# Kernel tuning notes

Hardware: AMD Instinct MI355X
Metric: run time of the kernel (lower is better)

## Reference

```python
import jax, jax.numpy as jnp
import numpy as np
from jax import lax

EPS = 1e-8


def setup_inputs() -> dict:
    key = jax.random.key(0)
    k1, k2, k3, k4, k5 = jax.random.split(key, 5)
    b, c_in, c_out, h, w_sp, k, z = 8, 256, 256, 128, 128, 3, 512
    return {
        "x": jax.random.normal(k1, (b, c_in, h, w_sp), dtype=jnp.float32),
        "w": jax.random.normal(k2, (b, z), dtype=jnp.float32),
        "weight": jax.random.normal(k3, (c_out, c_in, k, k), dtype=jnp.float32),
        "affine_w": jax.random.normal(k4, (c_in, z), dtype=jnp.float32) * 0.02,
        "affine_b": jax.random.normal(k5, (c_in,), dtype=jnp.float32) * 0.02,
    }


def reference(x, w, weight, affine_w, affine_b):
    # style: [b, c_in] -> broadcast over (out_ch, kh, kw); +1 as in StyleGAN2
    style = w @ affine_w.T + affine_b + 1.0                      # [b, c_in]
    wgt = weight[None] * style[:, None, :, None, None]           # [b, O, I, kh, kw]
    # demodulation
    denom = lax.rsqrt(jnp.sum(wgt * wgt, axis=(2, 3, 4)) + EPS)  # [b, O]
    wgt = wgt * denom[:, :, None, None, None]

    # per-sample conv (equivalent to groups=b grouped conv), 'same' padding
    def conv_one(xi, wi):
        # xi: [I, H, W], wi: [O, I, kh, kw]
        return lax.conv_general_dilated(
            xi[None], wi, window_strides=(1, 1), padding="SAME",
            dimension_numbers=("NCHW", "OIHW", "NCHW"))[0]

    return jax.vmap(conv_one)(x, wgt)                            # [b, O, H, W]
```

## Files before the change

### kernel.cpp

```cpp
#include <hip/hip_runtime.h>

#define EPS 1e-8f

using short8 = __attribute__((ext_vector_type(8))) short;
using f32x16 = __attribute__((ext_vector_type(16))) float;
typedef unsigned short u16;

#define WAITV(N) asm volatile("s_waitcnt vmcnt(" #N ")" ::: "memory")
#define BARRIER() do { __builtin_amdgcn_s_barrier(); \
                       asm volatile("" ::: "memory"); } while (0)

__device__ __forceinline__ u16 f2bf(float f) {
    union { float f; unsigned u; } v; v.f = f;
    unsigned u = v.u;
    return (u16)((u + 0x7FFFu + ((u >> 16) & 1u)) >> 16);
}

__device__ __forceinline__ void g2l16(const void* gsrc, void* ldst) {
    __builtin_amdgcn_global_load_lds(
        (const __attribute__((address_space(1))) unsigned int*)gsrc,
        (__attribute__((address_space(3))) unsigned int*)ldst, 16, 0, 0);
}

__global__ void style_kernel(const float* __restrict__ w,
                             const float* __restrict__ affine_w,
                             const float* __restrict__ affine_b,
                             float* __restrict__ style) {
    int b = blockIdx.x;
    int i = threadIdx.x;
    __shared__ float wb[512];
    for (int z = threadIdx.x; z < 512; z += 256) wb[z] = w[b * 512 + z];
    __syncthreads();
    const float* aw = affine_w + i * 512;
    float acc = 0.f;
#pragma unroll 4
    for (int z = 0; z < 512; z += 4) {
        float4 a4 = *reinterpret_cast<const float4*>(aw + z);
        acc += a4.x * wb[z] + a4.y * wb[z + 1] + a4.z * wb[z + 2] + a4.w * wb[z + 3];
    }
    style[b * 256 + i] = acc + affine_b[i] + 1.0f;
}

__global__ void modw_kernel(const float* __restrict__ weight,
                            const float* __restrict__ style,
                            u16* __restrict__ wgt) {
    int b = blockIdx.x >> 8;
    int o = blockIdx.x & 255;
    int ic = threadIdx.x;
    float s = style[b * 256 + ic];
    const float* wp = weight + (size_t)(o * 256 + ic) * 9;
    float m[9];
    float ss = 0.f;
#pragma unroll
    for (int t = 0; t < 9; ++t) { m[t] = wp[t] * s; ss += m[t] * m[t]; }
#pragma unroll
    for (int off = 32; off > 0; off >>= 1) ss += __shfl_down(ss, off);
    __shared__ float part[4];
    int lane = threadIdx.x & 63, wid = threadIdx.x >> 6;
    if (lane == 0) part[wid] = ss;
    __syncthreads();
    float denom = rsqrtf(part[0] + part[1] + part[2] + part[3] + EPS);
    int g = ic >> 3, j = ic & 7;
#pragma unroll
    for (int t = 0; t < 9; ++t) {
        size_t idx = ((((size_t)(b * 9 + t) * 32 + g) * 256 + o) << 3) + j;
        wgt[idx] = f2bf(m[t] * denom);
    }
}

__global__ __launch_bounds__(256) void xform_kernel(const float* __restrict__ x,
                                                    u16* __restrict__ xb) {
    int s = blockIdx.x * 256 + threadIdx.x;
    int w = s & 127, h = (s >> 7) & 127, g = (s >> 14) & 31, b = s >> 19;
    const float* xp = x + (((size_t)(b * 256 + g * 8) * 128 + h) * 128 + w);
    union { u16 u[8]; short8 v; } pk;
#pragma unroll
    for (int j = 0; j < 8; ++j) pk.u[j] = f2bf(xp[(size_t)j * 16384]);
    *reinterpret_cast<short8*>(&xb[(size_t)s * 8]) = pk.v;
}

__global__ __launch_bounds__(256, 2) void conv_kernel(
    const u16* __restrict__ xb,
    const u16* __restrict__ wgt,
    float* __restrict__ out) {

    __shared__ __align__(16) u16 Xs[2][4][4][130][8];
    __shared__ __align__(16) u16 trash[1024];

    int bid = blockIdx.x;
    int swz = (bid & 7) * 128 + (bid >> 3);
    int ht = swz & 63, ot = (swz >> 6) & 1, b = swz >> 7;
    int h0 = ht * 2;

    int tid = threadIdx.x, lane = tid & 63, wid = tid >> 6;
    int wm = wid >> 1, wr = wid & 1;
    int l31 = lane & 31, lh = lane >> 5;

    int hr = h0 + wid - 1;
    bool hValid = ((unsigned)hr < 128u);
    int hc = hValid ? hr : 0;

    const u16* aBase = wgt + ((size_t)(b * 9) * 32 * 256 +
                              (size_t)(lh * 256 + ot * 128 + wm * 64 + l31)) * 8;

    auto loadA = [&](short8 dst[2][2], int c, int t) {
#pragma unroll
        for (int kk = 0; kk < 2; ++kk)
#pragma unroll
            for (int mi = 0; mi < 2; ++mi)
                dst[kk][mi] = *reinterpret_cast<const short8*>(
                    aBase + (size_t)(((t * 32) + c * 4 + kk * 2) * 256 + mi * 32) * 8);
    };
    auto stageX = [&](int c1, int bx) {
#pragma unroll
        for (int k = 0; k < 8; ++k) {
            int g = k >> 1, half = k & 1;
            const u16* src = xb +
                ((((size_t)(b * 32 + c1 * 4 + g)) * 128 + hc) * 128 + half * 64 + lane) * 8;
            void* dst = hValid ? (void*)&Xs[bx][wid][g][1 + half * 64][0] : (void*)trash;
            g2l16(src, dst);
        }
    };

    {
        short8 z = {0, 0, 0, 0, 0, 0, 0, 0};
        short8* p0 = reinterpret_cast<short8*>(&Xs[0][0][0][0][0]);
        for (int i = tid; i < 4160; i += 256) p0[i] = z;
    }
    __syncthreads();

    short8 afC[2][2], afN[2][2];
    stageX(0, 0);
    loadA(afC, 0, 0);
    WAITV(4);
    BARRIER();

    f32x16 acc[2][4] = {};

    for (int c = 0; c < 8; ++c) {
        int buf = c & 1;
#pragma unroll
        for (int t = 0; t < 9; ++t) {
            if (!(c == 7 && t == 8))
                loadA(afN, t < 8 ? c : c + 1, t < 8 ? t + 1 : 0);
            if (t == 0 && c < 7) stageX(c + 1, buf ^ 1);

            int kh = t / 3, kw = t - kh * 3;
            short8 bx8[2][4];
#pragma unroll
            for (int kk = 0; kk < 2; ++kk)
#pragma unroll
                for (int ni = 0; ni < 4; ++ni)
                    bx8[kk][ni] = *reinterpret_cast<const short8*>(
                        &Xs[buf][wr + kh][kk * 2 + lh][ni * 32 + l31 + kw][0]);
            __builtin_amdgcn_s_setprio(1);
#pragma unroll
            for (int mi = 0; mi < 2; ++mi)
#pragma unroll
                for (int ni = 0; ni < 4; ++ni)
#pragma unroll
                    for (int kk = 0; kk < 2; ++kk)
                        acc[mi][ni] = __builtin_amdgcn_mfma_f32_32x32x16_bf16(
                            afC[kk][mi], bx8[kk][ni], acc[mi][ni], 0, 0, 0);
            __builtin_amdgcn_s_setprio(0);
#pragma unroll
            for (int kk = 0; kk < 2; ++kk)
#pragma unroll
                for (int mi = 0; mi < 2; ++mi)
                    afC[kk][mi] = afN[kk][mi];
        }
        WAITV(4);
        BARRIER();
    }

    int h = h0 + wr;
#pragma unroll
    for (int mi = 0; mi < 2; ++mi) {
        int ob = ot * 128 + wm * 64 + mi * 32 + 4 * lh;
#pragma unroll
        for (int ni = 0; ni < 4; ++ni) {
            int w_ = ni * 32 + l31;
#pragma unroll
            for (int reg = 0; reg < 16; ++reg) {
                int o = ob + (reg & 3) + 8 * (reg >> 2);
                out[(((size_t)(b * 256 + o) * 128 + h) * 128) + w_] = acc[mi][ni][reg];
            }
        }
    }
}

extern "C" void kernel_launch(void* const* d_in, const int* in_sizes, int n_in,
                              void* d_out, int out_size, void* d_ws, size_t ws_size,
                              hipStream_t stream) {
    const float* x        = (const float*)d_in[0];
    const float* w        = (const float*)d_in[1];
    const float* weight   = (const float*)d_in[2];
    const float* affine_w = (const float*)d_in[3];
    const float* affine_b = (const float*)d_in[4];
    float* out = (float*)d_out;

    float* style = (float*)d_ws;
    u16* wgt = (u16*)((char*)d_ws + 8192);
    u16* xbuf = (u16*)((char*)d_ws + 8192 + 9437184);

    xform_kernel<<<16384, 256, 0, stream>>>(x, xbuf);
    style_kernel<<<8, 256, 0, stream>>>(w, affine_w, affine_b, style);
    modw_kernel<<<2048, 256, 0, stream>>>(weight, style, wgt);
    conv_kernel<<<1024, 256, 0, stream>>>(xbuf, wgt, out);
}
```

Baseline: 196.3 us.

## Software-pipeline LDS B-fragment loads at half-tap granularity in conv loop

Splits each 3x3 tap into two k-halves and double-buffers the B operand registers, loading the next half-tap's X fragments from LDS while the current eight MFMAs run. Weight prefetch and the next-chunk global-to-LDS staging move to the second half-step, and the final barrier after the last chunk is dropped. The goal is to hide LDS read latency behind MFMA work. It costs a few extra live registers and adds more complex scheduling, which could affect occupancy at launch bounds of 2 waves per SIMD.

```diff
diff --git a/kernel.cpp b/kernel.cpp
--- a/kernel.cpp
+++ b/kernel.cpp
@@ -136,41 +136,47 @@
     BARRIER();
 
     f32x16 acc[2][4] = {};
+    short8 bxb[2][4];
 
     for (int c = 0; c < 8; ++c) {
         int buf = c & 1;
 #pragma unroll
-        for (int t = 0; t < 9; ++t) {
-            if (!(c == 7 && t == 8))
+        for (int ni = 0; ni < 4; ++ni)
+            bxb[0][ni] = *reinterpret_cast<const short8*>(
+                &Xs[buf][wr][lh][ni * 32 + l31][0]);
+#pragma unroll
+        for (int hp = 0; hp < 18; ++hp) {
+            int t = hp >> 1, kk = hp & 1;
+            if (hp < 17) {
+                int hp2 = hp + 1, t2 = hp2 >> 1, kk2 = hp2 & 1;
+                int kh2 = t2 / 3, kw2 = t2 - kh2 * 3;
+#pragma unroll
+                for (int ni = 0; ni < 4; ++ni)
+                    bxb[hp2 & 1][ni] = *reinterpret_cast<const short8*>(
+                        &Xs[buf][wr + kh2][kk2 * 2 + lh][ni * 32 + l31 + kw2][0]);
+            }
+            if (kk == 1 && !(c == 7 && t == 8))
                 loadA(afN, t < 8 ? c : c + 1, t < 8 ? t + 1 : 0);
-            if (t == 0 && c < 7) stageX(c + 1, buf ^ 1);
-
-            int kh = t / 3, kw = t - kh * 3;
-            short8 bx8[2][4];
-#pragma unroll
-            for (int kk = 0; kk < 2; ++kk)
+            if (hp == 1 && c < 7) stageX(c + 1, buf ^ 1);
+
+            __builtin_amdgcn_s_setprio(1);
+#pragma unroll
+            for (int mi = 0; mi < 2; ++mi)
 #pragma unroll
                 for (int ni = 0; ni < 4; ++ni)
-                    bx8[kk][ni] = *reinterpret_cast<const short8*>(
-                        &Xs[buf][wr + kh][kk * 2 + lh][ni * 32 + l31 + kw][0]);
-            __builtin_amdgcn_s_setprio(1);
-#pragma unroll
-            for (int mi = 0; mi < 2; ++mi)
-#pragma unroll
-                for (int ni = 0; ni < 4; ++ni)
-#pragma unroll
-                    for (int kk = 0; kk < 2; ++kk)
-                        acc[mi][ni] = __builtin_amdgcn_mfma_f32_32x32x16_bf16(
-                            afC[kk][mi], bx8[kk][ni], acc[mi][ni], 0, 0, 0);
+                    acc[mi][ni] = __builtin_amdgcn_mfma_f32_32x32x16_bf16(
+                        afC[kk][mi], bxb[hp & 1][ni], acc[mi][ni], 0, 0, 0);
             __builtin_amdgcn_s_setprio(0);
-#pragma unroll
-            for (int kk = 0; kk < 2; ++kk)
-#pragma unroll
-                for (int mi = 0; mi < 2; ++mi)
-                    afC[kk][mi] = afN[kk][mi];
+
+            if (kk == 1 && !(c == 7 && t == 8)) {
+#pragma unroll
+                for (int k2 = 0; k2 < 2; ++k2)
+#pragma unroll
+                    for (int mi = 0; mi < 2; ++mi)
+                        afC[k2][mi] = afN[k2][mi];
+            }
         }
-        WAITV(4);
-        BARRIER();
+        if (c < 7) { WAITV(4); BARRIER(); }
     }
 
     int h = h0 + wr;
```

Measured after the change: 192.5 us. No clear change (-1.9%).

## Split conv block into eight waves with half-width tiles per wave

Applied to the files above, without the earlier changes.

Raises the conv kernel block from 256 to 512 threads. Each wave now computes a 64x64 output tile instead of 64x128, so the accumulator array halves. X staging is split across the eight waves by row and channel group, and B fragments are loaded per kk inside the MFMA loop to cut register pressure. This aims for more resident waves to hide latency, at the cost of each wave reloading the same A fragments (weights) twice as often per block, plus more barrier participants.

```diff
diff --git a/kernel.cpp b/kernel.cpp
--- a/kernel.cpp
+++ b/kernel.cpp
@@ -79,7 +79,7 @@
     *reinterpret_cast<short8*>(&xb[(size_t)s * 8]) = pk.v;
 }
 
-__global__ __launch_bounds__(256, 2) void conv_kernel(
+__global__ __launch_bounds__(512, 4) void conv_kernel(
     const u16* __restrict__ xb,
     const u16* __restrict__ wgt,
     float* __restrict__ out) {
@@ -93,10 +93,11 @@
     int h0 = ht * 2;
 
     int tid = threadIdx.x, lane = tid & 63, wid = tid >> 6;
-    int wm = wid >> 1, wr = wid & 1;
+    int wm = wid >> 2, wr = (wid >> 1) & 1, wn = wid & 1;
     int l31 = lane & 31, lh = lane >> 5;
 
-    int hr = h0 + wid - 1;
+    int srow = wid >> 1, gsel = wid & 1;
+    int hr = h0 + srow - 1;
     bool hValid = ((unsigned)hr < 128u);
     int hc = hValid ? hr : 0;
 
@@ -113,11 +114,11 @@
     };
     auto stageX = [&](int c1, int bx) {
 #pragma unroll
-        for (int k = 0; k < 8; ++k) {
-            int g = k >> 1, half = k & 1;
+        for (int k = 0; k < 4; ++k) {
+            int g = gsel * 2 + (k >> 1), half = k & 1;
             const u16* src = xb +
                 ((((size_t)(b * 32 + c1 * 4 + g)) * 128 + hc) * 128 + half * 64 + lane) * 8;
-            void* dst = hValid ? (void*)&Xs[bx][wid][g][1 + half * 64][0] : (void*)trash;
+            void* dst = hValid ? (void*)&Xs[bx][srow][g][1 + half * 64][0] : (void*)trash;
             g2l16(src, dst);
         }
     };
@@ -125,7 +126,7 @@
     {
         short8 z = {0, 0, 0, 0, 0, 0, 0, 0};
         short8* p0 = reinterpret_cast<short8*>(&Xs[0][0][0][0][0]);
-        for (int i = tid; i < 4160; i += 256) p0[i] = z;
+        for (int i = tid; i < 4160; i += 512) p0[i] = z;
     }
     __syncthreads();
 
@@ -135,42 +136,44 @@
     WAITV(4);
     BARRIER();
 
-    f32x16 acc[2][4] = {};
+    f32x16 acc[2][2] = {};
 
     for (int c = 0; c < 8; ++c) {
         int buf = c & 1;
 #pragma unroll
         for (int t = 0; t < 9; ++t) {
-            if (!(c == 7 && t == 8))
+            bool lastTap = (c == 7 && t == 8);
+            if (!lastTap)
                 loadA(afN, t < 8 ? c : c + 1, t < 8 ? t + 1 : 0);
             if (t == 0 && c < 7) stageX(c + 1, buf ^ 1);
 
             int kh = t / 3, kw = t - kh * 3;
-            short8 bx8[2][4];
-#pragma unroll
-            for (int kk = 0; kk < 2; ++kk)
-#pragma unroll
-                for (int ni = 0; ni < 4; ++ni)
-                    bx8[kk][ni] = *reinterpret_cast<const short8*>(
-                        &Xs[buf][wr + kh][kk * 2 + lh][ni * 32 + l31 + kw][0]);
             __builtin_amdgcn_s_setprio(1);
 #pragma unroll
-            for (int mi = 0; mi < 2; ++mi)
-#pragma unroll
-                for (int ni = 0; ni < 4; ++ni)
-#pragma unroll
-                    for (int kk = 0; kk < 2; ++kk)
+            for (int kk = 0; kk < 2; ++kk) {
+                short8 bxv[2];
+#pragma unroll
+                for (int ni = 0; ni < 2; ++ni)
+                    bxv[ni] = *reinterpret_cast<const short8*>(
+                        &Xs[buf][wr + kh][kk * 2 + lh][wn * 64 + ni * 32 + l31 + kw][0]);
+#pragma unroll
+                for (int mi = 0; mi < 2; ++mi)
+#pragma unroll
+                    for (int ni = 0; ni < 2; ++ni)
                         acc[mi][ni] = __builtin_amdgcn_mfma_f32_32x32x16_bf16(
-                            afC[kk][mi], bx8[kk][ni], acc[mi][ni], 0, 0, 0);
+                            afC[kk][mi], bxv[ni], acc[mi][ni], 0, 0, 0);
+            }
             __builtin_amdgcn_s_setprio(0);
-#pragma unroll
-            for (int kk = 0; kk < 2; ++kk)
-#pragma unroll
-                for (int mi = 0; mi < 2; ++mi)
-                    afC[kk][mi] = afN[kk][mi];
+
+            if (!lastTap) {
+#pragma unroll
+                for (int k2 = 0; k2 < 2; ++k2)
+#pragma unroll
+                    for (int mi = 0; mi < 2; ++mi)
+                        afC[k2][mi] = afN[k2][mi];
+            }
         }
-        WAITV(4);
-        BARRIER();
+        if (c < 7) { WAITV(4); BARRIER(); }
     }
 
     int h = h0 + wr;
@@ -178,8 +181,8 @@
     for (int mi = 0; mi < 2; ++mi) {
         int ob = ot * 128 + wm * 64 + mi * 32 + 4 * lh;
 #pragma unroll
-        for (int ni = 0; ni < 4; ++ni) {
-            int w_ = ni * 32 + l31;
+        for (int ni = 0; ni < 2; ++ni) {
+            int w_ = wn * 64 + ni * 32 + l31;
 #pragma unroll
             for (int reg = 0; reg < 16; ++reg) {
                 int o = ob + (reg & 3) + 8 * (reg >> 2);
@@ -206,5 +209,5 @@
     xform_kernel<<<16384, 256, 0, stream>>>(x, xbuf);
     style_kernel<<<8, 256, 0, stream>>>(w, affine_w, affine_b, style);
     modw_kernel<<<2048, 256, 0, stream>>>(weight, style, wgt);
-    conv_kernel<<<1024, 256, 0, stream>>>(xbuf, wgt, out);
-}
+    conv_kernel<<<1024, 512, 0, stream>>>(xbuf, wgt, out);
+}
```

After: 209.7 us. 1.07x slower.

## Fuse fp32-to-bf16 input conversion into conv kernel with register-staged pipelining

Applied to the files above, without the earlier changes.

Removes the separate xform kernel, which converted x to channel-grouped bf16 in a workspace. The conv kernel now reads fp32 x directly into registers and converts to bf16 in place of the global_load_lds staging. The loads for the next channel chunk are spread across the nine taps, with one batch issued per tap and written to LDS on the following tap, to overlap with MFMA work. This saves a full read and write pass over x and one launch. In exchange, each x row is reloaded by every block that needs it (about twice, once per output-channel tile), register pressure rises, and stores go through VGPRs.

```diff
diff --git a/kernel.cpp b/kernel.cpp
--- a/kernel.cpp
+++ b/kernel.cpp
@@ -6,20 +6,14 @@
 using f32x16 = __attribute__((ext_vector_type(16))) float;
 typedef unsigned short u16;
 
-#define WAITV(N) asm volatile("s_waitcnt vmcnt(" #N ")" ::: "memory")
 #define BARRIER() do { __builtin_amdgcn_s_barrier(); \
                        asm volatile("" ::: "memory"); } while (0)
+#define LGKM0() asm volatile("s_waitcnt lgkmcnt(0)" ::: "memory")
 
 __device__ __forceinline__ u16 f2bf(float f) {
     union { float f; unsigned u; } v; v.f = f;
     unsigned u = v.u;
     return (u16)((u + 0x7FFFu + ((u >> 16) & 1u)) >> 16);
-}
-
-__device__ __forceinline__ void g2l16(const void* gsrc, void* ldst) {
-    __builtin_amdgcn_global_load_lds(
-        (const __attribute__((address_space(1))) unsigned int*)gsrc,
-        (__attribute__((address_space(3))) unsigned int*)ldst, 16, 0, 0);
 }
 
 __global__ void style_kernel(const float* __restrict__ w,
@@ -68,24 +62,12 @@
     }
 }
 
-__global__ __launch_bounds__(256) void xform_kernel(const float* __restrict__ x,
-                                                    u16* __restrict__ xb) {
-    int s = blockIdx.x * 256 + threadIdx.x;
-    int w = s & 127, h = (s >> 7) & 127, g = (s >> 14) & 31, b = s >> 19;
-    const float* xp = x + (((size_t)(b * 256 + g * 8) * 128 + h) * 128 + w);
-    union { u16 u[8]; short8 v; } pk;
-#pragma unroll
-    for (int j = 0; j < 8; ++j) pk.u[j] = f2bf(xp[(size_t)j * 16384]);
-    *reinterpret_cast<short8*>(&xb[(size_t)s * 8]) = pk.v;
-}
-
 __global__ __launch_bounds__(256, 2) void conv_kernel(
-    const u16* __restrict__ xb,
+    const float* __restrict__ x,
     const u16* __restrict__ wgt,
     float* __restrict__ out) {
 
     __shared__ __align__(16) u16 Xs[2][4][4][130][8];
-    __shared__ __align__(16) u16 trash[1024];
 
     int bid = blockIdx.x;
     int swz = (bid & 7) * 128 + (bid >> 3);
@@ -102,6 +84,7 @@
 
     const u16* aBase = wgt + ((size_t)(b * 9) * 32 * 256 +
                               (size_t)(lh * 256 + ot * 128 + wm * 64 + l31)) * 8;
+    const float* xBase = x + ((size_t)(b * 256) * 128 + hc) * 128;
 
     auto loadA = [&](short8 dst[2][2], int c, int t) {
 #pragma unroll
@@ -111,15 +94,18 @@
                 dst[kk][mi] = *reinterpret_cast<const short8*>(
                     aBase + (size_t)(((t * 32) + c * 4 + kk * 2) * 256 + mi * 32) * 8);
     };
-    auto stageX = [&](int c1, int bx) {
-#pragma unroll
-        for (int k = 0; k < 8; ++k) {
-            int g = k >> 1, half = k & 1;
-            const u16* src = xb +
-                ((((size_t)(b * 32 + c1 * 4 + g)) * 128 + hc) * 128 + half * 64 + lane) * 8;
-            void* dst = hValid ? (void*)&Xs[bx][wid][g][1 + half * 64][0] : (void*)trash;
-            g2l16(src, dst);
-        }
+    auto issueX = [&](float* dst, int c1, int bt) {
+        int g = bt >> 1, half = bt & 1;
+        const float* sp = xBase + (size_t)(c1 * 32 + g * 8) * 16384 + half * 64 + lane;
+#pragma unroll
+        for (int j = 0; j < 8; ++j) dst[j] = sp[(size_t)j * 16384];
+    };
+    auto writeX = [&](const float* src, int bt, int bx) {
+        int g = bt >> 1, half = bt & 1;
+        union { u16 u[8]; short8 v; } pk;
+#pragma unroll
+        for (int j = 0; j < 8; ++j) pk.u[j] = f2bf(src[j]);
+        *reinterpret_cast<short8*>(&Xs[bx][wid][g][1 + half * 64 + lane][0]) = pk.v;
     };
 
     {
@@ -130,20 +116,32 @@
     __syncthreads();
 
     short8 afC[2][2], afN[2][2];
-    stageX(0, 0);
+    if (hValid) {
+        float xg0[8][8];
+#pragma unroll
+        for (int bt = 0; bt < 8; ++bt) issueX(xg0[bt], 0, bt);
+#pragma unroll
+        for (int bt = 0; bt < 8; ++bt) writeX(xg0[bt], bt, 0);
+    }
     loadA(afC, 0, 0);
-    WAITV(4);
+    LGKM0();
     BARRIER();
 
     f32x16 acc[2][4] = {};
+    float xg[2][8];
 
     for (int c = 0; c < 8; ++c) {
         int buf = c & 1;
+        bool stage = (c < 7) && hValid;
 #pragma unroll
         for (int t = 0; t < 9; ++t) {
-            if (!(c == 7 && t == 8))
+            bool lastTap = (c == 7 && t == 8);
+            if (!lastTap)
                 loadA(afN, t < 8 ? c : c + 1, t < 8 ? t + 1 : 0);
-            if (t == 0 && c < 7) stageX(c + 1, buf ^ 1);
+            if (stage) {
+                if (t < 8) issueX(xg[t & 1], c + 1, t);
+                if (t > 0) writeX(xg[(t - 1) & 1], t - 1, buf ^ 1);
+            }
 
             int kh = t / 3, kw = t - kh * 3;
             short8 bx8[2][4];
@@ -163,14 +161,16 @@
                         acc[mi][ni] = __builtin_amdgcn_mfma_f32_32x32x16_bf16(
                             afC[kk][mi], bx8[kk][ni], acc[mi][ni], 0, 0, 0);
             __builtin_amdgcn_s_setprio(0);
-#pragma unroll
-            for (int kk = 0; kk < 2; ++kk)
-#pragma unroll
-                for (int mi = 0; mi < 2; ++mi)
-                    afC[kk][mi] = afN[kk][mi];
+
+            if (!lastTap) {
+#pragma unroll
+                for (int k2 = 0; k2 < 2; ++k2)
+#pragma unroll
+                    for (int mi = 0; mi < 2; ++mi)
+                        afC[k2][mi] = afN[k2][mi];
+            }
         }
-        WAITV(4);
-        BARRIER();
+        if (c < 7) { LGKM0(); BARRIER(); }
     }
 
     int h = h0 + wr;
@@ -201,10 +201,8 @@
 
     float* style = (float*)d_ws;
     u16* wgt = (u16*)((char*)d_ws + 8192);
-    u16* xbuf = (u16*)((char*)d_ws + 8192 + 9437184);
-
-    xform_kernel<<<16384, 256, 0, stream>>>(x, xbuf);
+
     style_kernel<<<8, 256, 0, stream>>>(w, affine_w, affine_b, style);
     modw_kernel<<<2048, 256, 0, stream>>>(weight, style, wgt);
-    conv_kernel<<<1024, 256, 0, stream>>>(xbuf, wgt, out);
-}
+    conv_kernel<<<1024, 256, 0, stream>>>(x, wgt, out);
+}
```

Measured after the change: 183.7 us. 1.07x faster.
